# Kernel optimization log

Measured on AMD Instinct MI355X. Metric: run time of the kernel, lower is better.

The kernel has to match this reference:

```python
import jax, jax.numpy as jnp
import numpy as np

N = 100000
E = 1600000
IN_F = 128
OUT_F = 64
ALPHA = 0.2  # leaky relu slope
EPS = 1e-16


def setup_inputs() -> dict:
    key = jax.random.key(0)
    k1, k2, k3, k4 = jax.random.split(key, 4)
    x = jax.random.normal(k1, (N, IN_F), dtype=jnp.float32)
    edge_index = jax.random.randint(k2, (2, E), 0, N, dtype=jnp.int64)
    # xavier_uniform with gain=1.414
    gain = 1.414
    limW = gain * np.sqrt(6.0 / (IN_F + OUT_F))
    W = jax.random.uniform(k3, (IN_F, OUT_F), minval=-limW, maxval=limW, dtype=jnp.float32)
    lima = gain * np.sqrt(6.0 / (2 * OUT_F + 1))
    a = jax.random.uniform(k4, (2 * OUT_F, 1), minval=-lima, maxval=lima, dtype=jnp.float32)
    return {"x": x, "edge_index": edge_index, "W": W, "a": a}


def reference(x, edge_index, W, a):
    src = edge_index[0]
    tgt = edge_index[1]
    Wh = x @ W  # (N, out)
    # e = leakyrelu([Wh[src] || Wh[tgt]] @ a) ; split a to avoid materializing concat
    a_src = a[:OUT_F, 0]
    a_tgt = a[OUT_F:, 0]
    score_src = Wh @ a_src  # (N,)
    score_tgt = Wh @ a_tgt  # (N,)
    e = jax.nn.leaky_relu(score_src[src] + score_tgt[tgt], ALPHA)  # (E,)
    # segment softmax over edges grouped by target node
    e_max = jax.ops.segment_max(e, tgt, num_segments=N)  # -inf for empty segments, never gathered
    e_exp = jnp.exp(e - e_max[tgt])
    e_sum = jax.ops.segment_sum(e_exp, tgt, num_segments=N)
    alpha = e_exp / (e_sum[tgt] + EPS)  # (E,)
    # dropout is identity in eval mode
    v_weighted = Wh[src] * alpha[:, None]  # (E, out)
    h_prime = jax.ops.segment_sum(v_weighted, tgt, num_segments=N)  # (N, out)
    return jax.nn.elu(h_prime)  # concat=True branch
```

## Files before the change

kernel.cpp:

```cpp
#include <hip/hip_runtime.h>

#define N_NODES 100000
#define N_EDGES 1600000
#define IN_FEAT 128
#define OUT_FEAT 64
#define LRELU_SLOPE 0.2f
#define EPS_DENOM 1e-16f

#define SB_SHIFT 8
#define SB_NODES 256
#define NSB 391
#define N_SUB 8
#define SUBA_CAP 704
#define STAGE_CAP 4608
#define CH 4096
#define SCAT_BLOCKS ((N_EDGES + CH - 1) / CH)
#define GEMM_BLOCKS ((N_NODES + 63) / 64)

typedef __attribute__((ext_vector_type(8))) short bf16x8;
typedef __attribute__((ext_vector_type(4))) float f32x4;

__device__ __forceinline__ unsigned int enc_f(float x) {
    unsigned int u = __float_as_uint(x);
    return (u & 0x80000000u) ? ~u : (u | 0x80000000u);
}
__device__ __forceinline__ float dec_f(unsigned int u) {
    u = (u & 0x80000000u) ? (u ^ 0x80000000u) : ~u;
    return __uint_as_float(u);
}
#define ENC_NEG_INF 0x007FFFFFu

__device__ __forceinline__ unsigned short f2bf(float f) {
    unsigned int u = __float_as_uint(f);
    u = (u + 0x7FFFu + ((u >> 16) & 1u)) >> 16;
    return (unsigned short)u;
}

__global__ __launch_bounds__(256) void init_prep_kernel(
    const float* __restrict__ W, int* __restrict__ cursorA,
    unsigned short* __restrict__ WTb)
{
    const int i = blockIdx.x * 256 + threadIdx.x;
    if (i < NSB * N_SUB) cursorA[i] = i * SUBA_CAP;
    if (i < OUT_FEAT * IN_FEAT) {
        const int n = i >> 7, k = i & 127;
        WTb[i] = f2bf(W[k * OUT_FEAT + n]);
    }
}

struct GemmS {
    unsigned short xs[64][136];
    float ssp[4][64];
    float stp[4][64];
};
struct ScatS {
    int staged[CH];
    int hcnt[NSB];
    int gbase[NSB];
    int lcnt[NSB];
    int lbase[NSB];
    int pfx[256];
};

__global__ __launch_bounds__(256) void gemm_scatter_kernel(
    const float* __restrict__ x, const unsigned short* __restrict__ WTb,
    const float* __restrict__ a, const int* __restrict__ ei,
    int* __restrict__ cursorA, int* __restrict__ bucketsA,
    unsigned short* __restrict__ WhB,
    float* __restrict__ s_src, float* __restrict__ s_tgt)
{
    __shared__ __align__(16) char smem[sizeof(ScatS) > sizeof(GemmS) ? sizeof(ScatS)
                                                                     : sizeof(GemmS)];
    const int tid = threadIdx.x;

    if (blockIdx.x < SCAT_BLOCKS) {
        ScatS& S = *(ScatS*)smem;
        const int base = blockIdx.x * CH;
        const int sub = blockIdx.x & (N_SUB - 1);
        for (int j = tid; j < NSB; j += 256) S.hcnt[j] = 0;
        __syncthreads();
        int tloc[CH / 256], sloc[CH / 256];
        #pragma unroll
        for (int k = 0; k < CH / 256; ++k) {
            const int i = base + k * 256 + tid;
            tloc[k] = (i < N_EDGES) ? ei[N_EDGES + i] : -1;
            sloc[k] = (i < N_EDGES) ? ei[i] : 0;
            if (tloc[k] >= 0) atomicAdd(&S.hcnt[tloc[k] >> SB_SHIFT], 1);
        }
        __syncthreads();
        int carry = 0;
        for (int c0 = 0; c0 < NSB; c0 += 256) {
            const int idx = c0 + tid;
            const int v = (idx < NSB) ? S.hcnt[idx] : 0;
            int incl = v;
            #pragma unroll
            for (int off = 1; off < 64; off <<= 1) {
                const int t = __shfl_up(incl, off, 64);
                if ((tid & 63) >= off) incl += t;
            }
            if ((tid & 63) == 63) S.pfx[tid >> 6] = incl;
            __syncthreads();
            int wpre = 0;
            for (int wv = 0; wv < (tid >> 6); ++wv) wpre += S.pfx[wv];
            if (idx < NSB) S.lbase[idx] = carry + wpre + incl - v;
            carry += S.pfx[0] + S.pfx[1] + S.pfx[2] + S.pfx[3];
            __syncthreads();
        }
        for (int j = tid; j < NSB; j += 256) {
            S.lcnt[j] = 0;
            const int c = S.hcnt[j];
            S.gbase[j] = c ? atomicAdd(&cursorA[j * N_SUB + sub], c) : 0;
        }
        __syncthreads();
        #pragma unroll
        for (int k = 0; k < CH / 256; ++k) {
            if (tloc[k] >= 0) {
                const int sb = tloc[k] >> SB_SHIFT;
                const int r = atomicAdd(&S.lcnt[sb], 1);
                S.staged[S.lbase[sb] + r] = sloc[k] | ((tloc[k] & (SB_NODES - 1)) << 17);
            }
        }
        __syncthreads();
        const int grp = tid >> 4, gl = tid & 15;
        for (int sb = grp; sb < NSB; sb += 16) {
            const int c = S.hcnt[sb];
            const int lb = S.lbase[sb];
            const int gb = S.gbase[sb];
            for (int k = gl; k < c; k += 16) bucketsA[gb + k] = S.staged[lb + k];
        }
        return;
    }

    GemmS& G = *(GemmS*)smem;
    const int wid = tid >> 6, lane = tid & 63;
    const int r0 = (blockIdx.x - SCAT_BLOCKS) * 64;

    #pragma unroll
    for (int it = 0; it < 8; ++it) {
        const int idx4 = it * 256 + tid;
        const int row = idx4 >> 5;
        const int col = (idx4 & 31) * 4;
        float4 v = make_float4(0.f, 0.f, 0.f, 0.f);
        if (r0 + row < N_NODES) v = *(const float4*)(x + (size_t)(r0 + row) * IN_FEAT + col);
        const unsigned int p0 = (unsigned int)f2bf(v.x) | ((unsigned int)f2bf(v.y) << 16);
        const unsigned int p1 = (unsigned int)f2bf(v.z) | ((unsigned int)f2bf(v.w) << 16);
        *(uint2*)&G.xs[row][col] = make_uint2(p0, p1);
    }
    __syncthreads();

    const int cgrp = lane >> 4;
    const int cl = lane & 15;
    const int col = wid * 16 + cl;
    f32x4 acc0 = {0.f,0.f,0.f,0.f}, acc1 = acc0, acc2 = acc0, acc3 = acc0;
    #pragma unroll
    for (int kb = 0; kb < IN_FEAT; kb += 32) {
        const bf16x8 bfrag = *(const bf16x8*)(WTb + col * IN_FEAT + kb + cgrp * 8);
        const bf16x8 a0 = *(const bf16x8*)&G.xs[ 0 + cl][kb + cgrp * 8];
        const bf16x8 a1 = *(const bf16x8*)&G.xs[16 + cl][kb + cgrp * 8];
        const bf16x8 a2 = *(const bf16x8*)&G.xs[32 + cl][kb + cgrp * 8];
        const bf16x8 a3 = *(const bf16x8*)&G.xs[48 + cl][kb + cgrp * 8];
        acc0 = __builtin_amdgcn_mfma_f32_16x16x32_bf16(a0, bfrag, acc0, 0, 0, 0);
        acc1 = __builtin_amdgcn_mfma_f32_16x16x32_bf16(a1, bfrag, acc1, 0, 0, 0);
        acc2 = __builtin_amdgcn_mfma_f32_16x16x32_bf16(a2, bfrag, acc2, 0, 0, 0);
        acc3 = __builtin_amdgcn_mfma_f32_16x16x32_bf16(a3, bfrag, acc3, 0, 0, 0);
    }

    const float a_s = a[col], a_t = a[OUT_FEAT + col];
    #pragma unroll
    for (int mt = 0; mt < 4; ++mt) {
        const f32x4 av = (mt == 0) ? acc0 : (mt == 1) ? acc1 : (mt == 2) ? acc2 : acc3;
        #pragma unroll
        for (int r = 0; r < 4; ++r) {
            const int lrow = mt * 16 + cgrp * 4 + r;
            const float v = av[r];
            const int grow = r0 + lrow;
            if (grow < N_NODES) WhB[(size_t)grow * OUT_FEAT + col] = f2bf(v);
            float ss = v * a_s;
            float st = v * a_t;
            #pragma unroll
            for (int off = 1; off < 16; off <<= 1) {
                ss += __shfl_xor(ss, off, 64);
                st += __shfl_xor(st, off, 64);
            }
            if (cl == 0) { G.ssp[wid][lrow] = ss; G.stp[wid][lrow] = st; }
        }
    }
    __syncthreads();
    if (tid < 64 && r0 + tid < N_NODES) {
        s_src[r0 + tid] = (G.ssp[0][tid] + G.ssp[1][tid]) + (G.ssp[2][tid] + G.ssp[3][tid]);
        s_tgt[r0 + tid] = (G.stp[0][tid] + G.stp[1][tid]) + (G.stp[2][tid] + G.stp[3][tid]);
    }
}

__global__ __launch_bounds__(512) void sort_aggr_kernel(
    const int* __restrict__ cursorA, const int* __restrict__ bucketsA,
    const float* __restrict__ s_src, const float* __restrict__ s_tgt,
    const unsigned short* __restrict__ WhB, float* __restrict__ out)
{
    __shared__ int2 sorted[STAGE_CAP];
    __shared__ float stgt[SB_NODES];
    __shared__ int cnt[SB_NODES];
    __shared__ int pfx[SB_NODES];
    __shared__ int cur[SB_NODES];
    __shared__ unsigned int m_enc[SB_NODES];
    __shared__ int scnt[N_SUB];
    __shared__ int wsum[4];
    const int b = blockIdx.x;
    const int tid = threadIdx.x;

    if (tid < SB_NODES) {
        cnt[tid] = 0;
        m_enc[tid] = ENC_NEG_INF;
        const int node = b * SB_NODES + tid;
        stgt[tid] = (node < N_NODES) ? s_tgt[node] : 0.0f;
    }
    if (tid < N_SUB) scnt[tid] = cursorA[b * N_SUB + tid] - (b * N_SUB + tid) * SUBA_CAP;
    __syncthreads();

    #pragma unroll
    for (int s = 0; s < N_SUB; ++s) {
        const int c = scnt[s];
        const int* src = bucketsA + (size_t)(b * N_SUB + s) * SUBA_CAP;
        for (int k = tid; k < c; k += 512) {
            const int pk = src[k];
            const int tl = (pk >> 17) & (SB_NODES - 1);
            float v = s_src[pk & 0x1FFFF] + stgt[tl];
            v = (v >= 0.0f) ? v : LRELU_SLOPE * v;
            atomicAdd(&cnt[tl], 1);
            atomicMax(&m_enc[tl], enc_f(v));
        }
    }
    __syncthreads();

    int vv = 0, incl = 0;
    if (tid < SB_NODES) {
        vv = cnt[tid];
        incl = vv;
        #pragma unroll
        for (int off = 1; off < 64; off <<= 1) {
            const int t = __shfl_up(incl, off, 64);
            if ((tid & 63) >= off) incl += t;
        }
        if ((tid & 63) == 63) wsum[tid >> 6] = incl;
    }
    __syncthreads();
    if (tid < SB_NODES) {
        int wpre = 0;
        for (int wv = 0; wv < (tid >> 6); ++wv) wpre += wsum[wv];
        const int ex = wpre + incl - vv;
        pfx[tid] = ex;
        cur[tid] = ex;
    }
    __syncthreads();

    #pragma unroll
    for (int s = 0; s < N_SUB; ++s) {
        const int c = scnt[s];
        const int* src = bucketsA + (size_t)(b * N_SUB + s) * SUBA_CAP;
        for (int k = tid; k < c; k += 512) {
            const int pk = src[k];
            const int tl = (pk >> 17) & (SB_NODES - 1);
            float v = s_src[pk & 0x1FFFF] + stgt[tl];
            v = (v >= 0.0f) ? v : LRELU_SLOPE * v;
            const int pos = atomicAdd(&cur[tl], 1);
            const float w = __expf(v - dec_f(m_enc[tl]));
            sorted[pos] = make_int2(pk & 0x1FFFF, __float_as_int(w));
        }
    }
    __syncthreads();

    const int grp = tid >> 4, gl = tid & 15;
    const char* whb = (const char*)WhB;
    const unsigned int foff = (unsigned int)gl << 3;
    #pragma unroll
    for (int n = 0; n < 8; ++n) {
        const int nl = grp * 8 + n;
        const int node = b * SB_NODES + nl;
        if (node >= N_NODES) continue;
        const int beg = pfx[nl];
        const int end = beg + cnt[nl];
        float a0 = 0.f, a1 = 0.f, a2 = 0.f, a3 = 0.f, sum = 0.f;
        int i = beg;
        for (; i + 4 <= end; i += 4) {
            const int2 p0 = sorted[i],     p1 = sorted[i + 1];
            const int2 p2 = sorted[i + 2], p3 = sorted[i + 3];
            const uint2 g0 = *(const uint2*)(whb + (((unsigned int)p0.x << 7) + foff));
            const uint2 g1 = *(const uint2*)(whb + (((unsigned int)p1.x << 7) + foff));
            const uint2 g2 = *(const uint2*)(whb + (((unsigned int)p2.x << 7) + foff));
            const uint2 g3 = *(const uint2*)(whb + (((unsigned int)p3.x << 7) + foff));
            const float w0 = __int_as_float(p0.y), w1 = __int_as_float(p1.y);
            const float w2 = __int_as_float(p2.y), w3 = __int_as_float(p3.y);
            a0 += w0 * __uint_as_float(g0.x << 16) + w1 * __uint_as_float(g1.x << 16)
                + w2 * __uint_as_float(g2.x << 16) + w3 * __uint_as_float(g3.x << 16);
            a1 += w0 * __uint_as_float(g0.x & 0xFFFF0000u) + w1 * __uint_as_float(g1.x & 0xFFFF0000u)
                + w2 * __uint_as_float(g2.x & 0xFFFF0000u) + w3 * __uint_as_float(g3.x & 0xFFFF0000u);
            a2 += w0 * __uint_as_float(g0.y << 16) + w1 * __uint_as_float(g1.y << 16)
                + w2 * __uint_as_float(g2.y << 16) + w3 * __uint_as_float(g3.y << 16);
            a3 += w0 * __uint_as_float(g0.y & 0xFFFF0000u) + w1 * __uint_as_float(g1.y & 0xFFFF0000u)
                + w2 * __uint_as_float(g2.y & 0xFFFF0000u) + w3 * __uint_as_float(g3.y & 0xFFFF0000u);
            sum += (w0 + w1) + (w2 + w3);
        }
        for (; i < end; ++i) {
            const int2 pk = sorted[i];
            const uint2 g0 = *(const uint2*)(whb + (((unsigned int)pk.x << 7) + foff));
            const float w0 = __int_as_float(pk.y);
            a0 += w0 * __uint_as_float(g0.x << 16);
            a1 += w0 * __uint_as_float(g0.x & 0xFFFF0000u);
            a2 += w0 * __uint_as_float(g0.y << 16);
            a3 += w0 * __uint_as_float(g0.y & 0xFFFF0000u);
            sum += w0;
        }
        const float inv = 1.0f / (sum + EPS_DENOM);
        float4 o;
        o.x = a0 * inv; o.y = a1 * inv; o.z = a2 * inv; o.w = a3 * inv;
        o.x = (o.x > 0.f) ? o.x : expm1f(o.x);
        o.y = (o.y > 0.f) ? o.y : expm1f(o.y);
        o.z = (o.z > 0.f) ? o.z : expm1f(o.z);
        o.w = (o.w > 0.f) ? o.w : expm1f(o.w);
        *(float4*)(out + (size_t)node * OUT_FEAT + (gl << 2)) = o;
    }
}

extern "C" void kernel_launch(void* const* d_in, const int* in_sizes, int n_in,
                              void* d_out, int out_size, void* d_ws, size_t ws_size,
                              hipStream_t stream) {
    const float* x  = (const float*)d_in[0];
    const int*   ei = (const int*)d_in[1];
    const float* W  = (const float*)d_in[2];
    const float* a  = (const float*)d_in[3];
    float* out = (float*)d_out;

    char* p = (char*)d_ws;
    unsigned short* WhB = (unsigned short*)p; p += (size_t)N_NODES * OUT_FEAT * 2;
    unsigned short* WTb = (unsigned short*)p; p += (size_t)OUT_FEAT * IN_FEAT * 2;
    float* s_src    = (float*)p;  p += (size_t)N_NODES * 4;
    float* s_tgt    = (float*)p;  p += (size_t)N_NODES * 4;
    int*   cursorA  = (int*)p;    p += (size_t)NSB * N_SUB * 4;
    p = (char*)(((size_t)p + 15) & ~(size_t)15);
    int*   bucketsA = (int*)p;    p += (size_t)NSB * N_SUB * SUBA_CAP * 4;

    init_prep_kernel<<<32, 256, 0, stream>>>(W, cursorA, WTb);
    gemm_scatter_kernel<<<SCAT_BLOCKS + GEMM_BLOCKS, 256, 0, stream>>>(
        x, WTb, a, ei, cursorA, bucketsA, WhB, s_src, s_tgt);
    sort_aggr_kernel<<<NSB, 512, 0, stream>>>(cursorA, bucketsA, s_src, s_tgt, WhB, out);
}
```

Before: 101.4 us.

## Halve supernode size and cache edge scores in LDS to skip second global pass

Supernodes shrink from 256 to 128 nodes, which doubles the number of sort/aggregate blocks to 782 and cuts per-bucket capacities. The first pass now stores each packed edge and its leaky-relu score in an LDS staging array. The second pass reads them from there instead of re-reading bucketsA and s_src from global memory and recomputing the score. This adds an LDS array and more scatter buckets, which raises bucket-overflow risk and scatter-side atomics in exchange for more parallelism and less global traffic.

```diff
diff --git a/kernel.cpp b/kernel.cpp
--- a/kernel.cpp
+++ b/kernel.cpp
@@ -7,12 +7,12 @@
 #define LRELU_SLOPE 0.2f
 #define EPS_DENOM 1e-16f
 
-#define SB_SHIFT 8
-#define SB_NODES 256
-#define NSB 391
+#define SB_SHIFT 7
+#define SB_NODES 128
+#define NSB 782
 #define N_SUB 8
-#define SUBA_CAP 704
-#define STAGE_CAP 4608
+#define SUBA_CAP 384
+#define STAGE_CAP 2432
 #define CH 4096
 #define SCAT_BLOCKS ((N_EDGES + CH - 1) / CH)
 #define GEMM_BLOCKS ((N_NODES + 63) / 64)
@@ -121,12 +121,12 @@
             }
         }
         __syncthreads();
-        const int grp = tid >> 4, gl = tid & 15;
-        for (int sb = grp; sb < NSB; sb += 16) {
+        const int grp = tid >> 3, gl = tid & 7;
+        for (int sb = grp; sb < NSB; sb += 32) {
             const int c = S.hcnt[sb];
             const int lb = S.lbase[sb];
             const int gb = S.gbase[sb];
-            for (int k = gl; k < c; k += 16) bucketsA[gb + k] = S.staged[lb + k];
+            for (int k = gl; k < c; k += 8) bucketsA[gb + k] = S.staged[lb + k];
         }
         return;
     }
@@ -197,14 +197,15 @@
     const float* __restrict__ s_src, const float* __restrict__ s_tgt,
     const unsigned short* __restrict__ WhB, float* __restrict__ out)
 {
+    __shared__ int2 stage[STAGE_CAP];
     __shared__ int2 sorted[STAGE_CAP];
     __shared__ float stgt[SB_NODES];
     __shared__ int cnt[SB_NODES];
     __shared__ int pfx[SB_NODES];
     __shared__ int cur[SB_NODES];
     __shared__ unsigned int m_enc[SB_NODES];
-    __shared__ int scnt[N_SUB];
-    __shared__ int wsum[4];
+    __shared__ int c_ofs[N_SUB + 1];
+    __shared__ int wsum[2];
     const int b = blockIdx.x;
     const int tid = threadIdx.x;
 
@@ -214,24 +215,33 @@
         const int node = b * SB_NODES + tid;
         stgt[tid] = (node < N_NODES) ? s_tgt[node] : 0.0f;
     }
-    if (tid < N_SUB) scnt[tid] = cursorA[b * N_SUB + tid] - (b * N_SUB + tid) * SUBA_CAP;
-    __syncthreads();
-
+    if (tid == 0) {
+        int o = 0;
+        #pragma unroll
+        for (int s = 0; s < N_SUB; ++s) {
+            c_ofs[s] = o;
+            o += cursorA[b * N_SUB + s] - (b * N_SUB + s) * SUBA_CAP;
+        }
+        c_ofs[N_SUB] = o;
+    }
+    __syncthreads();
+    const int tot = c_ofs[N_SUB];
     #pragma unroll
     for (int s = 0; s < N_SUB; ++s) {
-        const int c = scnt[s];
+        const int o = c_ofs[s];
+        const int c = c_ofs[s + 1] - o;
         const int* src = bucketsA + (size_t)(b * N_SUB + s) * SUBA_CAP;
         for (int k = tid; k < c; k += 512) {
             const int pk = src[k];
             const int tl = (pk >> 17) & (SB_NODES - 1);
             float v = s_src[pk & 0x1FFFF] + stgt[tl];
             v = (v >= 0.0f) ? v : LRELU_SLOPE * v;
+            stage[o + k] = make_int2(pk, __float_as_int(v));
             atomicAdd(&cnt[tl], 1);
             atomicMax(&m_enc[tl], enc_f(v));
         }
     }
     __syncthreads();
-
     int vv = 0, incl = 0;
     if (tid < SB_NODES) {
         vv = cnt[tid];
@@ -245,27 +255,18 @@
     }
     __syncthreads();
     if (tid < SB_NODES) {
-        int wpre = 0;
-        for (int wv = 0; wv < (tid >> 6); ++wv) wpre += wsum[wv];
+        const int wpre = (tid >= 64) ? wsum[0] : 0;
         const int ex = wpre + incl - vv;
         pfx[tid] = ex;
         cur[tid] = ex;
     }
     __syncthreads();
-
-    #pragma unroll
-    for (int s = 0; s < N_SUB; ++s) {
-        const int c = scnt[s];
-        const int* src = bucketsA + (size_t)(b * N_SUB + s) * SUBA_CAP;
-        for (int k = tid; k < c; k += 512) {
-            const int pk = src[k];
-            const int tl = (pk >> 17) & (SB_NODES - 1);
-            float v = s_src[pk & 0x1FFFF] + stgt[tl];
-            v = (v >= 0.0f) ? v : LRELU_SLOPE * v;
-            const int pos = atomicAdd(&cur[tl], 1);
-            const float w = __expf(v - dec_f(m_enc[tl]));
-            sorted[pos] = make_int2(pk & 0x1FFFF, __float_as_int(w));
-        }
+    for (int i = tid; i < tot; i += 512) {
+        const int2 pk = stage[i];
+        const int tl = (pk.x >> 17) & (SB_NODES - 1);
+        const int pos = atomicAdd(&cur[tl], 1);
+        const float w = __expf(__int_as_float(pk.y) - dec_f(m_enc[tl]));
+        sorted[pos] = make_int2(pk.x & 0x1FFFF, __float_as_int(w));
     }
     __syncthreads();
 
@@ -273,8 +274,8 @@
     const char* whb = (const char*)WhB;
     const unsigned int foff = (unsigned int)gl << 3;
     #pragma unroll
-    for (int n = 0; n < 8; ++n) {
-        const int nl = grp * 8 + n;
+    for (int n = 0; n < 4; ++n) {
+        const int nl = grp * 4 + n;
         const int node = b * SB_NODES + nl;
         if (node >= N_NODES) continue;
         const int beg = pfx[nl];
```

New measurement: 112.3 us. 10.8% more time.
